# Performance work log

Hardware: AMD Instinct MI355X
Metric: run time of the kernel (lower is better)

Reference implementation:

```python
import jax, jax.numpy as jnp
import numpy as np

B, S, E, H, V, C = 64, 512, 256, 128, 50000, 2


def setup_inputs() -> dict:
    key = jax.random.key(0)
    ks = jax.random.split(key, 12)
    sentences = jax.random.randint(ks[0], (B, S), 0, V, dtype=jnp.int32)
    # sparse binary adjacency (dependency-tree-like), float for bmm
    adj = (jax.random.uniform(ks[1], (B, S, S)) < 0.05).astype(jnp.float32)
    emb_table = jax.random.normal(ks[2], (V, E), dtype=jnp.float32) * 0.02
    W1 = jax.random.normal(ks[3], (H, E), dtype=jnp.float32) * 0.05
    b1 = jnp.zeros((H,), jnp.float32)
    W2 = jax.random.normal(ks[4], (H, H), dtype=jnp.float32) * 0.05
    b2 = jnp.zeros((H,), jnp.float32)
    W3 = jax.random.normal(ks[5], (H, H), dtype=jnp.float32) * 0.05
    b3 = jnp.zeros((H,), jnp.float32)
    Wp = jax.random.normal(ks[6], (C, H), dtype=jnp.float32) * 0.05
    bp = jnp.zeros((C,), jnp.float32)
    return {"sentences": sentences, "adj": adj, "emb_table": emb_table,
            "W1": W1, "b1": b1, "W2": W2, "b2": b2, "W3": W3, "b3": b3,
            "Wp": Wp, "bp": bp}


def reference(sentences, adj, emb_table, W1, b1, W2, b2, W3, b3, Wp, bp):
    # embedding lookup (dropout is eval-mode identity)
    h = emb_table[sentences]  # [B, S, E]
    # degree normalization term (self-loop adds +1)
    deg = jnp.sum(adj, axis=-1, keepdims=True) + 1.0  # [B, S, 1]
    for W, b in ((W1, b1), (W2, b2), (W3, b3)):
        agg = jnp.einsum('bst,btd->bsd', adj, h)  # bmm(adj, h)
        # layer(agg) + layer(h) == (agg + h) @ W^T + 2b  (shared weights)
        h = ((agg + h) @ W.T + 2.0 * b) / deg
        h = jax.nn.relu(h)
    # AdaptiveMaxPool1d(1) over sequence dim
    pooled = jnp.max(h, axis=1)  # [B, H]
    logits = pooled @ Wp.T + bp  # [B, C]
    return logits
```

## Files before the change

### kernel.cpp

```cpp
#include <hip/hip_runtime.h>
#include <hip/hip_bf16.h>

typedef unsigned short ushort_t;

#define B_ 64
#define S_ 512
#define E_ 256
#define H_ 128
#define M_ (B_ * S_)
#define CAP_ 128


__global__ void k_adjidx(const float* __restrict__ adj,
                         ushort_t* __restrict__ idxl,
                         int* __restrict__ nnz,
                         float* __restrict__ invdeg) {
    int row  = blockIdx.x * 4 + (threadIdx.x >> 6);
    int lane = threadIdx.x & 63;
    const float4* arow = (const float4*)(adj + (size_t)row * S_);
    ushort_t* dst = idxl + (size_t)row * CAP_;
    int total = 0;
    #pragma unroll
    for (int c = 0; c < 2; ++c) {
        float4 v = arow[c * 64 + lane];
        float f[4] = {v.x, v.y, v.z, v.w};
        #pragma unroll
        for (int j = 0; j < 4; ++j) {
            unsigned long long m = __ballot(f[j] != 0.0f);
            if (f[j] != 0.0f) {
                int pos = total + __popcll(m & ((1ull << lane) - 1ull));
                if (pos < CAP_) dst[pos] = (ushort_t)(c * 256 + lane * 4 + j);
            }
            total += __popcll(m);
        }
    }
    if (lane == 0) {
        nnz[row] = total < CAP_ ? total : CAP_;
        invdeg[row] = 1.0f / (float)(total + 1);
    }
}

template <int WSTRIDE, int XSTRIDE, bool GATHER, bool ADD>
__global__ __launch_bounds__(256, 2) void k_gemm(const float* __restrict__ X,
                                                 const int* __restrict__ sent,
                                                 const float* __restrict__ emb,
                                                 const float* __restrict__ W,
                                                 int kBase,
                                                 float* __restrict__ out) {
    __shared__ float Ws[128][68];
    __shared__ float Xs[4][16][36];
    int tid  = threadIdx.x;
    int wave = tid >> 6, lane = tid & 63;
    int rb       = blockIdx.x >> 1;
    int colBase  = (blockIdx.x & 1) * 64;
    int rowBase  = rb * 128 + wave * 32;

    {
        int j  = tid & 63;
        int kq = tid >> 6;
        const float* wp = W + (size_t)(colBase + j) * WSTRIDE + kBase + kq * 32;
        #pragma unroll
        for (int i = 0; i < 8; ++i) {
            float4 v = *(const float4*)(wp + i * 4);
            int k = kq * 32 + i * 4;
            Ws[k + 0][j] = v.x; Ws[k + 1][j] = v.y;
            Ws[k + 2][j] = v.z; Ws[k + 3][j] = v.w;
        }
    }

    int cc = lane & 15, rr = lane >> 4;
    int kg = lane & 3,  rowi = lane >> 2;

    const float* xs0;
    const float* xs1;
    if (GATHER) {
        xs0 = emb + (size_t)sent[rowBase + rowi]      * XSTRIDE + kBase + kg * 4;
        xs1 = emb + (size_t)sent[rowBase + rowi + 16] * XSTRIDE + kBase + kg * 4;
    } else {
        xs0 = X + (size_t)(rowBase + rowi)      * XSTRIDE + kBase + kg * 4;
        xs1 = X + (size_t)(rowBase + rowi + 16) * XSTRIDE + kBase + kg * 4;
    }
    float4 f0 = *(const float4*)(xs0);
    float4 f1 = *(const float4*)(xs1);

    __syncthreads();

    float acc[8][4] = {};
    float (*xsw)[36] = Xs[wave];

    #pragma unroll 1
    for (int kk = 0; kk < 128; kk += 16) {
        xsw[kg * 4 + 0][rowi] = f0.x; xsw[kg * 4 + 1][rowi] = f0.y;
        xsw[kg * 4 + 2][rowi] = f0.z; xsw[kg * 4 + 3][rowi] = f0.w;
        xsw[kg * 4 + 0][rowi + 16] = f1.x; xsw[kg * 4 + 1][rowi + 16] = f1.y;
        xsw[kg * 4 + 2][rowi + 16] = f1.z; xsw[kg * 4 + 3][rowi + 16] = f1.w;
        if (kk + 16 < 128) {
            f0 = *(const float4*)(xs0 + kk + 16);
            f1 = *(const float4*)(xs1 + kk + 16);
        }
        #pragma unroll
        for (int k = 0; k < 16; ++k) {
            float4 x0 = *(const float4*)&xsw[k][rr * 8];
            float4 x1 = *(const float4*)&xsw[k][rr * 8 + 4];
            float4 wv = *(const float4*)&Ws[kk + k][cc * 4];
            float xv[8] = {x0.x, x0.y, x0.z, x0.w, x1.x, x1.y, x1.z, x1.w};
            #pragma unroll
            for (int i = 0; i < 8; ++i) {
                acc[i][0] += xv[i] * wv.x;
                acc[i][1] += xv[i] * wv.y;
                acc[i][2] += xv[i] * wv.z;
                acc[i][3] += xv[i] * wv.w;
            }
        }
    }

    int col   = colBase + cc * 4;
    int chunk = col >> 5, jc = col & 31;
    #pragma unroll
    for (int i = 0; i < 8; ++i) {
        int row = rowBase + rr * 8 + i;
        int bb  = row >> 9, r = row & 511;
        float* op = out + (((size_t)bb * 4 + chunk) * 512 + r) * 32 + jc;
        float4 o = {acc[i][0], acc[i][1], acc[i][2], acc[i][3]};
        if (ADD) {
            float4 p = *(const float4*)op;
            o.x += p.x; o.y += p.y; o.z += p.z; o.w += p.w;
        }
        *(float4*)op = o;
    }
}

template <bool POOL>
__global__ __launch_bounds__(512) void k_aggf(const float* __restrict__ Y,
                                              const ushort_t* __restrict__ idxl,
                                              const int* __restrict__ nnz,
                                              const float* __restrict__ invdeg,
                                              const float* __restrict__ bias,
                                              float* __restrict__ out) {
    __shared__ float slab[512 * 32];
    float4* s4 = (float4*)slab;
    int b = blockIdx.x >> 2, chunk = blockIdx.x & 3;

    const float4* g4 = (const float4*)(Y + (((size_t)b * 4 + chunk) * 512) * 32);
    #pragma unroll
    for (int i = 0; i < 8; ++i) s4[threadIdx.x + i * 512] = g4[threadIdx.x + i * 512];
    __syncthreads();

    int lane = threadIdx.x & 63, wave = threadIdx.x >> 6;
    int grp  = wave * 8 + (lane >> 3);
    int j    = lane & 7;
    float4 bv = ((const float4*)bias)[chunk * 8 + j];
    bv.x *= 2.0f; bv.y *= 2.0f; bv.z *= 2.0f; bv.w *= 2.0f;

    float4 vmax = {-1e30f, -1e30f, -1e30f, -1e30f};

    #pragma unroll 1
    for (int i = 0; i < 8; ++i) {
        int r   = grp * 8 + i;
        int row = b * S_ + r;
        int n = nnz[row];
        const ushort_t* il = idxl + (size_t)row * CAP_;
        float4 acc = s4[r * 8 + j];
        float4 acc2 = {0.f, 0.f, 0.f, 0.f};
        int q = 0;
        for (; q + 4 <= n; q += 4) {
            int t0 = il[q], t1 = il[q + 1], t2 = il[q + 2], t3 = il[q + 3];
            float4 v0 = s4[t0 * 8 + j];
            float4 v1 = s4[t1 * 8 + j];
            float4 v2 = s4[t2 * 8 + j];
            float4 v3 = s4[t3 * 8 + j];
            acc.x += v0.x + v1.x; acc.y += v0.y + v1.y;
            acc.z += v0.z + v1.z; acc.w += v0.w + v1.w;
            acc2.x += v2.x + v3.x; acc2.y += v2.y + v3.y;
            acc2.z += v2.z + v3.z; acc2.w += v2.w + v3.w;
        }
        for (; q < n; ++q) {
            float4 v = s4[il[q] * 8 + j];
            acc.x += v.x; acc.y += v.y; acc.z += v.z; acc.w += v.w;
        }
        acc.x += acc2.x; acc.y += acc2.y; acc.z += acc2.z; acc.w += acc2.w;

        float inv = invdeg[row];
        float4 o;
        o.x = fmaxf((acc.x + bv.x) * inv, 0.0f);
        o.y = fmaxf((acc.y + bv.y) * inv, 0.0f);
        o.z = fmaxf((acc.z + bv.z) * inv, 0.0f);
        o.w = fmaxf((acc.w + bv.w) * inv, 0.0f);

        if (!POOL) {
            *(float4*)(out + (size_t)row * H_ + chunk * 32 + j * 4) = o;
        } else {
            vmax.x = fmaxf(vmax.x, o.x); vmax.y = fmaxf(vmax.y, o.y);
            vmax.z = fmaxf(vmax.z, o.z); vmax.w = fmaxf(vmax.w, o.w);
        }
    }

    if (POOL) {
        __syncthreads();
        s4[grp * 8 + j] = vmax;
        __syncthreads();
        if (threadIdx.x < 32) {
            int c = threadIdx.x;
            float m = -1e30f;
            #pragma unroll 8
            for (int g = 0; g < 64; ++g) m = fmaxf(m, slab[g * 32 + c]);
            out[(size_t)b * H_ + chunk * 32 + c] = m;
        }
    }
}

__global__ void k_final(const float* __restrict__ pooled,
                        const float* __restrict__ Wp,
                        const float* __restrict__ bp,
                        float* __restrict__ out) {
    int b = blockIdx.x, j = threadIdx.x;
    float m = pooled[(size_t)b * H_ + j];
    float t0 = m * Wp[j];
    float t1 = m * Wp[H_ + j];
    #pragma unroll
    for (int off = 32; off > 0; off >>= 1) {
        t0 += __shfl_down(t0, off);
        t1 += __shfl_down(t1, off);
    }
    __shared__ float red[2][2];
    int wave = j >> 6, lane = j & 63;
    if (lane == 0) { red[0][wave] = t0; red[1][wave] = t1; }
    __syncthreads();
    if (j == 0) out[b * 2 + 0] = red[0][0] + red[0][1] + bp[0];
    if (j == 1) out[b * 2 + 1] = red[1][0] + red[1][1] + bp[1];
}

extern "C" void kernel_launch(void* const* d_in, const int* in_sizes, int n_in,
                              void* d_out, int out_size, void* d_ws, size_t ws_size,
                              hipStream_t stream) {
    const int*   sent = (const int*)d_in[0];
    const float* adj  = (const float*)d_in[1];
    const float* emb  = (const float*)d_in[2];
    const float* W1   = (const float*)d_in[3];
    const float* b1   = (const float*)d_in[4];
    const float* W2   = (const float*)d_in[5];
    const float* b2   = (const float*)d_in[6];
    const float* W3   = (const float*)d_in[7];
    const float* b3   = (const float*)d_in[8];
    const float* Wp   = (const float*)d_in[9];
    const float* bp   = (const float*)d_in[10];
    float* out = (float*)d_out;

    char* ws = (char*)d_ws;
    float*    bufA   = (float*)ws;
    float*    bufB   = (float*)(ws + (size_t)M_ * 256 * 4);
    float*    invdeg = (float*)(ws + (size_t)M_ * 512 * 4);
    int*      nnz    = (int*)(ws + (size_t)M_ * 512 * 4 + M_ * 4);
    ushort_t* idxl   = (ushort_t*)(ws + (size_t)M_ * 512 * 4 + M_ * 8);
    float*    pooled = (float*)(ws + (size_t)M_ * 512 * 4 + M_ * 8 + (size_t)M_ * CAP_ * 2);

    k_adjidx<<<M_ / 4, 256, 0, stream>>>(adj, idxl, nnz, invdeg);

    k_gemm<E_, E_, true, false><<<512, 256, 0, stream>>>(nullptr, sent, emb, W1, 0,   bufA);
    k_gemm<E_, E_, true, true ><<<512, 256, 0, stream>>>(nullptr, sent, emb, W1, 128, bufA);
    k_aggf<false><<<B_ * 4, 512, 0, stream>>>(bufA, idxl, nnz, invdeg, b1, bufB);

    k_gemm<H_, H_, false, false><<<512, 256, 0, stream>>>(bufB, nullptr, nullptr, W2, 0, bufA);
    k_aggf<false><<<B_ * 4, 512, 0, stream>>>(bufA, idxl, nnz, invdeg, b2, bufB);

    k_gemm<H_, H_, false, false><<<512, 256, 0, stream>>>(bufB, nullptr, nullptr, W3, 0, bufA);
    k_aggf<true><<<B_ * 4, 512, 0, stream>>>(bufA, idxl, nnz, invdeg, b3, pooled);

    k_final<<<B_, H_, 0, stream>>>(pooled, Wp, bp, out);
}
```

Baseline: 306.5 us.

## Fuse K-halves in GEMM and narrow aggregation slabs to 16 columns with XCD mapping

The first-layer GEMM now loops over both K halves in one kernel instead of two launches with a read-modify-write accumulate. The intermediate layout changes from 4 chunks of 32 columns to 8 chunks of 16, so each aggregation block stages a smaller padded (stride 17) LDS slab. It runs 512 blocks of 256 threads with one scalar column per lane and a prefetched neighbour index. Block indices are remapped so each XCD handles a fixed set of batches, aiming for better occupancy and L2 locality, at the cost of scalar rather than float4 LDS gathers.

```diff
diff --git a/kernel.cpp b/kernel.cpp
--- a/kernel.cpp
+++ b/kernel.cpp
@@ -40,33 +40,19 @@
     }
 }
 
-template <int WSTRIDE, int XSTRIDE, bool GATHER, bool ADD>
+template <int K, bool GATHER>
 __global__ __launch_bounds__(256, 2) void k_gemm(const float* __restrict__ X,
                                                  const int* __restrict__ sent,
                                                  const float* __restrict__ emb,
                                                  const float* __restrict__ W,
-                                                 int kBase,
                                                  float* __restrict__ out) {
-    __shared__ float Ws[128][68];
-    __shared__ float Xs[4][16][36];
+    __shared__ float Ws[128 * 68];
+    __shared__ float Xs[4][16 * 36];
     int tid  = threadIdx.x;
     int wave = tid >> 6, lane = tid & 63;
-    int rb       = blockIdx.x >> 1;
-    int colBase  = (blockIdx.x & 1) * 64;
-    int rowBase  = rb * 128 + wave * 32;
-
-    {
-        int j  = tid & 63;
-        int kq = tid >> 6;
-        const float* wp = W + (size_t)(colBase + j) * WSTRIDE + kBase + kq * 32;
-        #pragma unroll
-        for (int i = 0; i < 8; ++i) {
-            float4 v = *(const float4*)(wp + i * 4);
-            int k = kq * 32 + i * 4;
-            Ws[k + 0][j] = v.x; Ws[k + 1][j] = v.y;
-            Ws[k + 2][j] = v.z; Ws[k + 3][j] = v.w;
-        }
-    }
+    int rb      = blockIdx.x >> 1;
+    int colBase = (blockIdx.x & 1) * 64;
+    int rowBase = rb * 128 + wave * 32;
 
     int cc = lane & 15, rr = lane >> 4;
     int kg = lane & 3,  rowi = lane >> 2;
@@ -74,137 +60,131 @@
     const float* xs0;
     const float* xs1;
     if (GATHER) {
-        xs0 = emb + (size_t)sent[rowBase + rowi]      * XSTRIDE + kBase + kg * 4;
-        xs1 = emb + (size_t)sent[rowBase + rowi + 16] * XSTRIDE + kBase + kg * 4;
+        xs0 = emb + (size_t)sent[rowBase + rowi]      * K + kg * 4;
+        xs1 = emb + (size_t)sent[rowBase + rowi + 16] * K + kg * 4;
     } else {
-        xs0 = X + (size_t)(rowBase + rowi)      * XSTRIDE + kBase + kg * 4;
-        xs1 = X + (size_t)(rowBase + rowi + 16) * XSTRIDE + kBase + kg * 4;
-    }
-    float4 f0 = *(const float4*)(xs0);
-    float4 f1 = *(const float4*)(xs1);
-
-    __syncthreads();
+        xs0 = X + (size_t)(rowBase + rowi)      * K + kg * 4;
+        xs1 = X + (size_t)(rowBase + rowi + 16) * K + kg * 4;
+    }
 
     float acc[8][4] = {};
-    float (*xsw)[36] = Xs[wave];
-
-    #pragma unroll 1
-    for (int kk = 0; kk < 128; kk += 16) {
-        xsw[kg * 4 + 0][rowi] = f0.x; xsw[kg * 4 + 1][rowi] = f0.y;
-        xsw[kg * 4 + 2][rowi] = f0.z; xsw[kg * 4 + 3][rowi] = f0.w;
-        xsw[kg * 4 + 0][rowi + 16] = f1.x; xsw[kg * 4 + 1][rowi + 16] = f1.y;
-        xsw[kg * 4 + 2][rowi + 16] = f1.z; xsw[kg * 4 + 3][rowi + 16] = f1.w;
-        if (kk + 16 < 128) {
-            f0 = *(const float4*)(xs0 + kk + 16);
-            f1 = *(const float4*)(xs1 + kk + 16);
-        }
-        #pragma unroll
-        for (int k = 0; k < 16; ++k) {
-            float4 x0 = *(const float4*)&xsw[k][rr * 8];
-            float4 x1 = *(const float4*)&xsw[k][rr * 8 + 4];
-            float4 wv = *(const float4*)&Ws[kk + k][cc * 4];
-            float xv[8] = {x0.x, x0.y, x0.z, x0.w, x1.x, x1.y, x1.z, x1.w};
+    float* xsw = Xs[wave];
+
+    for (int kh = 0; kh < K; kh += 128) {
+        if (kh) __syncthreads();
+        {
+            int j  = tid & 63;
+            int kq = tid >> 6;
+            const float* wp = W + (size_t)(colBase + j) * K + kh + kq * 32;
             #pragma unroll
             for (int i = 0; i < 8; ++i) {
-                acc[i][0] += xv[i] * wv.x;
-                acc[i][1] += xv[i] * wv.y;
-                acc[i][2] += xv[i] * wv.z;
-                acc[i][3] += xv[i] * wv.w;
+                float4 v = *(const float4*)(wp + i * 4);
+                int k = kq * 32 + i * 4;
+                Ws[(k + 0) * 68 + j] = v.x; Ws[(k + 1) * 68 + j] = v.y;
+                Ws[(k + 2) * 68 + j] = v.z; Ws[(k + 3) * 68 + j] = v.w;
+            }
+        }
+        float4 f0 = *(const float4*)(xs0 + kh);
+        float4 f1 = *(const float4*)(xs1 + kh);
+        __syncthreads();
+
+        #pragma unroll 1
+        for (int kk = 0; kk < 128; kk += 16) {
+            xsw[(kg * 4 + 0) * 36 + rowi] = f0.x;
+            xsw[(kg * 4 + 1) * 36 + rowi] = f0.y;
+            xsw[(kg * 4 + 2) * 36 + rowi] = f0.z;
+            xsw[(kg * 4 + 3) * 36 + rowi] = f0.w;
+            xsw[(kg * 4 + 0) * 36 + rowi + 16] = f1.x;
+            xsw[(kg * 4 + 1) * 36 + rowi + 16] = f1.y;
+            xsw[(kg * 4 + 2) * 36 + rowi + 16] = f1.z;
+            xsw[(kg * 4 + 3) * 36 + rowi + 16] = f1.w;
+            if (kk + 16 < 128) {
+                f0 = *(const float4*)(xs0 + kh + kk + 16);
+                f1 = *(const float4*)(xs1 + kh + kk + 16);
+            }
+            #pragma unroll
+            for (int k = 0; k < 16; ++k) {
+                float4 a0 = *(const float4*)&xsw[k * 36 + rr * 8];
+                float4 a1 = *(const float4*)&xsw[k * 36 + rr * 8 + 4];
+                float4 wv = *(const float4*)&Ws[(kk + k) * 68 + cc * 4];
+                float xv[8] = {a0.x, a0.y, a0.z, a0.w, a1.x, a1.y, a1.z, a1.w};
+                #pragma unroll
+                for (int i = 0; i < 8; ++i) {
+                    acc[i][0] += xv[i] * wv.x;
+                    acc[i][1] += xv[i] * wv.y;
+                    acc[i][2] += xv[i] * wv.z;
+                    acc[i][3] += xv[i] * wv.w;
+                }
             }
         }
     }
 
     int col   = colBase + cc * 4;
-    int chunk = col >> 5, jc = col & 31;
+    int chunk = col >> 4, jc = col & 15;
     #pragma unroll
     for (int i = 0; i < 8; ++i) {
         int row = rowBase + rr * 8 + i;
         int bb  = row >> 9, r = row & 511;
-        float* op = out + (((size_t)bb * 4 + chunk) * 512 + r) * 32 + jc;
         float4 o = {acc[i][0], acc[i][1], acc[i][2], acc[i][3]};
-        if (ADD) {
-            float4 p = *(const float4*)op;
-            o.x += p.x; o.y += p.y; o.z += p.z; o.w += p.w;
-        }
-        *(float4*)op = o;
+        *(float4*)(out + (((size_t)bb * 8 + chunk) * 512 + r) * 16 + jc) = o;
     }
 }
 
 template <bool POOL>
-__global__ __launch_bounds__(512) void k_aggf(const float* __restrict__ Y,
+__global__ __launch_bounds__(256) void k_aggf(const float* __restrict__ Y,
                                               const ushort_t* __restrict__ idxl,
                                               const int* __restrict__ nnz,
                                               const float* __restrict__ invdeg,
                                               const float* __restrict__ bias,
                                               float* __restrict__ out) {
-    __shared__ float slab[512 * 32];
-    float4* s4 = (float4*)slab;
-    int b = blockIdx.x >> 2, chunk = blockIdx.x & 3;
-
-    const float4* g4 = (const float4*)(Y + (((size_t)b * 4 + chunk) * 512) * 32);
-    #pragma unroll
-    for (int i = 0; i < 8; ++i) s4[threadIdx.x + i * 512] = g4[threadIdx.x + i * 512];
+    __shared__ float s[512 * 17];
+    __shared__ float red[256];
+    int blk  = blockIdx.x;
+    int xcd  = blk & 7, slot7 = blk >> 3;
+    int b    = xcd + 8 * (slot7 >> 3);
+    int ch   = slot7 & 7;
+    int tid  = threadIdx.x;
+
+    const float4* g4 = (const float4*)(Y + ((size_t)b * 8 + ch) * 512 * 16);
+    #pragma unroll
+    for (int i = 0; i < 8; ++i) {
+        int idx = tid + i * 256;
+        int r = idx >> 2, c4 = idx & 3;
+        *(float4*)&s[r * 17 + c4 * 4] = g4[idx];
+    }
     __syncthreads();
 
-    int lane = threadIdx.x & 63, wave = threadIdx.x >> 6;
-    int grp  = wave * 8 + (lane >> 3);
-    int j    = lane & 7;
-    float4 bv = ((const float4*)bias)[chunk * 8 + j];
-    bv.x *= 2.0f; bv.y *= 2.0f; bv.z *= 2.0f; bv.w *= 2.0f;
-
-    float4 vmax = {-1e30f, -1e30f, -1e30f, -1e30f};
+    int wave = tid >> 6, lane = tid & 63;
+    int slot = lane >> 4, col = lane & 15;
+    float b2 = 2.0f * bias[ch * 16 + col];
+    float vmax = -1e30f;
 
     #pragma unroll 1
-    for (int i = 0; i < 8; ++i) {
-        int r   = grp * 8 + i;
+    for (int it = 0; it < 32; ++it) {
+        int r   = wave * 128 + it * 4 + slot;
         int row = b * S_ + r;
-        int n = nnz[row];
+        int n   = nnz[row];
         const ushort_t* il = idxl + (size_t)row * CAP_;
-        float4 acc = s4[r * 8 + j];
-        float4 acc2 = {0.f, 0.f, 0.f, 0.f};
-        int q = 0;
-        for (; q + 4 <= n; q += 4) {
-            int t0 = il[q], t1 = il[q + 1], t2 = il[q + 2], t3 = il[q + 3];
-            float4 v0 = s4[t0 * 8 + j];
-            float4 v1 = s4[t1 * 8 + j];
-            float4 v2 = s4[t2 * 8 + j];
-            float4 v3 = s4[t3 * 8 + j];
-            acc.x += v0.x + v1.x; acc.y += v0.y + v1.y;
-            acc.z += v0.z + v1.z; acc.w += v0.w + v1.w;
-            acc2.x += v2.x + v3.x; acc2.y += v2.y + v3.y;
-            acc2.z += v2.z + v3.z; acc2.w += v2.w + v3.w;
-        }
-        for (; q < n; ++q) {
-            float4 v = s4[il[q] * 8 + j];
-            acc.x += v.x; acc.y += v.y; acc.z += v.z; acc.w += v.w;
-        }
-        acc.x += acc2.x; acc.y += acc2.y; acc.z += acc2.z; acc.w += acc2.w;
-
-        float inv = invdeg[row];
-        float4 o;
-        o.x = fmaxf((acc.x + bv.x) * inv, 0.0f);
-        o.y = fmaxf((acc.y + bv.y) * inv, 0.0f);
-        o.z = fmaxf((acc.z + bv.z) * inv, 0.0f);
-        o.w = fmaxf((acc.w + bv.w) * inv, 0.0f);
-
-        if (!POOL) {
-            *(float4*)(out + (size_t)row * H_ + chunk * 32 + j * 4) = o;
-        } else {
-            vmax.x = fmaxf(vmax.x, o.x); vmax.y = fmaxf(vmax.y, o.y);
-            vmax.z = fmaxf(vmax.z, o.z); vmax.w = fmaxf(vmax.w, o.w);
-        }
+        float acc = s[r * 17 + col];
+        int idx = (n > 0) ? il[0] : 0;
+        for (int t = 0; t < n; ++t) {
+            int nidx = (t + 1 < n) ? il[t + 1] : 0;
+            acc += s[idx * 17 + col];
+            idx = nidx;
+        }
+        float o = fmaxf((acc + b2) * invdeg[row], 0.0f);
+        if (POOL) vmax = fmaxf(vmax, o);
+        else      out[(size_t)row * H_ + ch * 16 + col] = o;
     }
 
     if (POOL) {
+        red[tid] = vmax;
         __syncthreads();
-        s4[grp * 8 + j] = vmax;
-        __syncthreads();
-        if (threadIdx.x < 32) {
-            int c = threadIdx.x;
-            float m = -1e30f;
-            #pragma unroll 8
-            for (int g = 0; g < 64; ++g) m = fmaxf(m, slab[g * 32 + c]);
-            out[(size_t)b * H_ + chunk * 32 + c] = m;
+        if (tid < 16) {
+            float m = red[tid];
+            #pragma unroll
+            for (int g = 1; g < 16; ++g) m = fmaxf(m, red[g * 16 + tid]);
+            out[(size_t)b * H_ + ch * 16 + tid] = m;
         }
     }
 }
@@ -247,24 +227,25 @@
     float* out = (float*)d_out;
 
     char* ws = (char*)d_ws;
-    float*    bufA   = (float*)ws;
-    float*    bufB   = (float*)(ws + (size_t)M_ * 256 * 4);
-    float*    invdeg = (float*)(ws + (size_t)M_ * 512 * 4);
-    int*      nnz    = (int*)(ws + (size_t)M_ * 512 * 4 + M_ * 4);
-    ushort_t* idxl   = (ushort_t*)(ws + (size_t)M_ * 512 * 4 + M_ * 8);
-    float*    pooled = (float*)(ws + (size_t)M_ * 512 * 4 + M_ * 8 + (size_t)M_ * CAP_ * 2);
+    float*    Ybuf   = (float*)ws;
+    float*    h1     = (float*)(ws + ((size_t)16 << 20));
+    float*    h2     = (float*)(ws + ((size_t)32 << 20));
+    char*     base   = ws + ((size_t)48 << 20);
+    float*    invdeg = (float*)base;
+    int*      nnz    = (int*)(base + (size_t)M_ * 4);
+    ushort_t* idxl   = (ushort_t*)(base + (size_t)M_ * 8);
+    float*    pooled = (float*)(base + (size_t)M_ * 8 + (size_t)M_ * CAP_ * 2);
 
     k_adjidx<<<M_ / 4, 256, 0, stream>>>(adj, idxl, nnz, invdeg);
 
-    k_gemm<E_, E_, true, false><<<512, 256, 0, stream>>>(nullptr, sent, emb, W1, 0,   bufA);
-    k_gemm<E_, E_, true, true ><<<512, 256, 0, stream>>>(nullptr, sent, emb, W1, 128, bufA);
-    k_aggf<false><<<B_ * 4, 512, 0, stream>>>(bufA, idxl, nnz, invdeg, b1, bufB);
-
-    k_gemm<H_, H_, false, false><<<512, 256, 0, stream>>>(bufB, nullptr, nullptr, W2, 0, bufA);
-    k_aggf<false><<<B_ * 4, 512, 0, stream>>>(bufA, idxl, nnz, invdeg, b2, bufB);
-
-    k_gemm<H_, H_, false, false><<<512, 256, 0, stream>>>(bufB, nullptr, nullptr, W3, 0, bufA);
-    k_aggf<true><<<B_ * 4, 512, 0, stream>>>(bufA, idxl, nnz, invdeg, b3, pooled);
+    k_gemm<E_, true ><<<512, 256, 0, stream>>>(nullptr, sent, emb, W1, Ybuf);
+    k_aggf<false><<<512, 256, 0, stream>>>(Ybuf, idxl, nnz, invdeg, b1, h1);
+
+    k_gemm<H_, false><<<512, 256, 0, stream>>>(h1, nullptr, nullptr, W2, Ybuf);
+    k_aggf<false><<<512, 256, 0, stream>>>(Ybuf, idxl, nnz, invdeg, b2, h2);
+
+    k_gemm<H_, false><<<512, 256, 0, stream>>>(h2, nullptr, nullptr, W3, Ybuf);
+    k_aggf<true ><<<512, 256, 0, stream>>>(Ybuf, idxl, nnz, invdeg, b3, pooled);
 
     k_final<<<B_, H_, 0, stream>>>(pooled, Wp, bp, out);
 }
```

Result: slower. 559.3 us (+82.5%).
